# Kernel optimization log

Hardware: AMD Instinct MI355X
Metric: run time of the kernel (lower is better)

## Reference

```python
import jax, jax.numpy as jnp
import numpy as np

B, S, H = 2, 2048, 2304
NH, NKV, HD = 8, 4, 256
SOFTCAP = 50.0
INIT = 0.02


def setup_inputs() -> dict:
    key = jax.random.key(0)
    k1, k2, k3, k4, k5 = jax.random.split(key, 5)
    hidden_states = jax.random.normal(k1, (B, S, H), dtype=jnp.float32)
    attention_mask = jnp.ones((B, S), dtype=jnp.int32)
    position_ids = jnp.broadcast_to(jnp.arange(S, dtype=jnp.int32), (B, S))
    Wq = jax.random.normal(k2, (H, NH * HD), dtype=jnp.float32) * INIT
    Wk = jax.random.normal(k3, (H, NKV * HD), dtype=jnp.float32) * INIT
    Wv = jax.random.normal(k4, (H, NKV * HD), dtype=jnp.float32) * INIT
    Wo = jax.random.normal(k5, (NH * HD, H), dtype=jnp.float32) * INIT
    return {"hidden_states": hidden_states, "attention_mask": attention_mask,
            "position_ids": position_ids, "Wq": Wq, "Wk": Wk, "Wv": Wv, "Wo": Wo}


def _rotate_half(t):
    return jnp.concatenate([-t[..., HD // 2:], t[..., :HD // 2]], axis=-1)


def reference(hidden_states, attention_mask, position_ids, Wq, Wk, Wv, Wo):
    b, s, _ = hidden_states.shape
    # projections + head split
    q = (hidden_states @ Wq).reshape(b, s, NH, HD)
    k = (hidden_states @ Wk).reshape(b, s, NKV, HD)
    v = (hidden_states @ Wv).reshape(b, s, NKV, HD)
    # RoPE (Gemma sinusoidal table, gathered by position_ids)
    inv_freq = 1.0 / (10000.0 ** (jnp.arange(0, HD, 2, dtype=jnp.float32) / HD))
    freqs = position_ids.astype(jnp.float32)[..., None] * inv_freq      # [B,S,HD/2]
    emb = jnp.concatenate([freqs, freqs], axis=-1)                      # [B,S,HD]
    sin = jnp.sin(emb)[:, :, None, :]
    cos = jnp.cos(emb)[:, :, None, :]
    q = q * cos + _rotate_half(q) * sin
    k = k * cos + _rotate_half(k) * sin
    # GQA: repeat KV heads to match query heads
    groups = NH // NKV
    k = jnp.repeat(k, groups, axis=2)
    v = jnp.repeat(v, groups, axis=2)
    # scaled logits, mask, tanh softcap (order matches source: mask -> softcap -> softmax)
    q = q / jnp.sqrt(jnp.float32(HD))
    scores = jnp.einsum('bqhd,bkhd->bhqk', q, k)                        # [B,NH,S,S]
    causal = jnp.tril(jnp.ones((s, s), dtype=bool))
    mask = causal[None, None] & (attention_mask[:, None, None, :] > 0)
    big_neg = jnp.finfo(scores.dtype).min
    scores = jnp.where(mask, scores, big_neg)
    scores = jnp.tanh(scores / SOFTCAP) * SOFTCAP
    w = jax.nn.softmax(scores, axis=-1)
    out = jnp.einsum('bhqk,bkhd->bqhd', w, v).reshape(b, s, NH * HD)
    return out @ Wo
```

## Files before the change

kernel.cpp:

```cpp
#include <hip/hip_runtime.h>
#include <hip/hip_bf16.h>
#include <stdint.h>

typedef unsigned short u16;
typedef __attribute__((ext_vector_type(8))) short s16x8;
typedef __attribute__((ext_vector_type(4))) float f32x4;

#define B_ 2
#define S_ 2048
#define H_ 2304
#define NH_ 8
#define NKV_ 4
#define HD_ 256

__device__ __forceinline__ float bf2f(u16 u) {
  union { uint32_t i; float f; } x; x.i = ((uint32_t)u) << 16; return x.f;
}
__device__ __forceinline__ u16 f2bf(float f) {
  union { float f; uint32_t i; } x; x.f = f;
  uint32_t u = x.i;
  return (u16)((u + 0x7fffu + ((u >> 16) & 1u)) >> 16);
}
__device__ __forceinline__ u16 f2bft(float f) {
  union { float f; uint32_t i; } x; x.f = f;
  return (u16)(x.i >> 16);
}

__device__ __forceinline__ void async16(const void* g, void* l) {
  __builtin_amdgcn_global_load_lds((const __attribute__((address_space(1))) uint32_t*)g,
                                   (__attribute__((address_space(3))) uint32_t*)l, 16, 0, 0);
}

__device__ __forceinline__ f32x4 mfma16(s16x8 a, s16x8 b, f32x4 c) {
  return __builtin_amdgcn_mfma_f32_16x16x32_bf16(a, b, c, 0, 0, 0);
}

__global__ __launch_bounds__(256) void prep_kernel(
    const float* __restrict__ X, u16* __restrict__ Xb,
    const float* __restrict__ Wq, u16* __restrict__ WqT,
    const float* __restrict__ Wk, u16* __restrict__ WkT,
    const float* __restrict__ Wv, u16* __restrict__ WvT,
    const float* __restrict__ Wo, u16* __restrict__ WoT,
    float* __restrict__ ct, float* __restrict__ st) {
  __shared__ u16 tile[32][33];
  int bid = blockIdx.x, tid = threadIdx.x;

  auto tposeT = [&](const float* in, u16* out, int R, int C, int bx, int by) {
    int c0 = bx * 32, r0 = by * 32;
    int x = tid & 31, y = tid >> 5;
#pragma unroll
    for (int j = 0; j < 32; j += 8)
      tile[y + j][x] = f2bf(in[(size_t)(r0 + y + j) * C + c0 + x]);
    __syncthreads();
#pragma unroll
    for (int j = 0; j < 32; j += 8)
      out[(size_t)(c0 + y + j) * R + r0 + x] = tile[x][y + j];
  };

  if (bid < 1024) {
    int t = bid * 256 + tid;
    int d = t & 127;
    int p = t >> 7;
    float invf = exp2f(-(float)d * 0.1038102530f);
    float f = (float)p * invf;
    float s, c;
    sincosf(f, &s, &c);
    ct[t] = c;
    st[t] = s;
  } else if (bid < 10240) {
    size_t i = ((size_t)(bid - 1024) * 256 + tid) * 4;
    float4 v = *(const float4*)(X + i);
    ushort4 o;
    o.x = f2bf(v.x); o.y = f2bf(v.y); o.z = f2bf(v.z); o.w = f2bf(v.w);
    *(ushort4*)(Xb + i) = o;
  } else if (bid < 14848) {
    int b2 = bid - 10240;
    tposeT(Wq, WqT, 2304, 2048, b2 & 63, b2 >> 6);
  } else if (bid < 17152) {
    int b2 = bid - 14848;
    tposeT(Wk, WkT, 2304, 1024, b2 & 31, b2 >> 5);
  } else if (bid < 19456) {
    int b2 = bid - 17152;
    tposeT(Wv, WvT, 2304, 1024, b2 & 31, b2 >> 5);
  } else {
    int b2 = bid - 19456;
    tposeT(Wo, WoT, 2048, 2304, b2 % 72, b2 / 72);
  }
}

__global__ __launch_bounds__(256) void mid_kernel(u16* __restrict__ QKV, u16* __restrict__ VTb,
                                                  const int* __restrict__ pos_ids,
                                                  const float* __restrict__ ct,
                                                  const float* __restrict__ st) {
  __shared__ u16 tile[32][33];
  int bid = blockIdx.x, tid = threadIdx.x;
  if (bid < 1024) {
    int t = bid * 256 + tid;
    int dg = t & 15, h = (t >> 4) & 3, row = t >> 6;
    u16* p1 = QKV + (size_t)row * 4096 + 2048 + h * 256 + dg * 8;
    u16* p2 = p1 + 128;
    int pos = pos_ids[row];
    const float* ctp = ct + pos * 128 + dg * 8;
    const float* stp = st + pos * 128 + dg * 8;
    s16x8 v1 = *(const s16x8*)p1, v2 = *(const s16x8*)p2;
#pragma unroll
    for (int j = 0; j < 8; j++) {
      float c = ctp[j], s = stp[j];
      float a = bf2f((u16)v1[j]);
      float b = bf2f((u16)v2[j]);
      v1[j] = (short)f2bf(a * c - b * s);
      v2[j] = (short)f2bf(b * c + a * s);
    }
    *(s16x8*)p1 = v1;
    *(s16x8*)p2 = v2;
  } else {
    int b2 = bid - 1024;
    int bx = b2 & 31;
    int by = (b2 >> 5) & 63;
    int z = b2 >> 11;
    const u16* in = QKV + 3072 + (size_t)z * 2048 * 4096;
    u16* out = VTb + (size_t)z * 1024 * 2048;
    int c0 = bx * 32, r0 = by * 32;
    int x = tid & 31, y = tid >> 5;
#pragma unroll
    for (int j = 0; j < 32; j += 8)
      tile[y + j][x] = in[(size_t)(r0 + y + j) * 4096 + c0 + x];
    __syncthreads();
#pragma unroll
    for (int j = 0; j < 32; j += 8)
      out[(size_t)(c0 + y + j) * 2048 + r0 + x] = tile[x][y + j];
  }
}

template <bool F32OUT>
__global__ __launch_bounds__(512) void gemm256(const u16* __restrict__ A, const u16* __restrict__ BT,
                                               void* __restrict__ Cout, int M, int N, int Kd) {
  __shared__ u16 As[2][256 * 64];
  __shared__ u16 Bs[2][256 * 64];
  int tid = threadIdx.x, lane = tid & 63, wave = tid >> 6;
  int nT = gridDim.x * gridDim.y;
  int bid = blockIdx.y * gridDim.x + blockIdx.x;
  int tile = (bid & 7) * (nT >> 3) + (bid >> 3);
  int bn = (tile % gridDim.x) * 256;
  int bm = (tile / gridDim.x) * 256;
  int wm = (wave >> 2) * 128, wn = (wave & 3) * 64;
  int fr = lane & 15, fq = lane >> 4;
  f32x4 acc[8][4];
#pragma unroll
  for (int i = 0; i < 8; i++)
#pragma unroll
    for (int j = 0; j < 4; j++) acc[i][j] = (f32x4){0.f, 0.f, 0.f, 0.f};

  int srow = tid >> 3, sslot = tid & 7;
  int scol = (sslot * 8) ^ ((srow & 7) << 3);
  const u16* Ab = A + (size_t)(bm + srow) * Kd + scol;
  const u16* Bb = BT + (size_t)(bn + srow) * Kd + scol;

  auto stage = [&](int buf, int k0) {
#pragma unroll
    for (int i = 0; i < 4; i++) {
      async16(Ab + (size_t)i * 64 * Kd + k0, (char*)&As[buf][0] + wave * 1024 + i * 8192);
      async16(Bb + (size_t)i * 64 * Kd + k0, (char*)&Bs[buf][0] + wave * 1024 + i * 8192);
    }
  };

  int NT = Kd >> 6;
  int rsw = (fr & 7) << 3;
  stage(0, 0);
  for (int t = 0; t < NT; ++t) {
    if (t + 1 < NT) {
      stage((t + 1) & 1, (t + 1) << 6);
      asm volatile("s_waitcnt vmcnt(8)" ::: "memory");
    } else {
      asm volatile("s_waitcnt vmcnt(0)" ::: "memory");
    }
    __builtin_amdgcn_sched_barrier(0);
    __builtin_amdgcn_s_barrier();
    __builtin_amdgcn_sched_barrier(0);
    const u16* Ap = &As[t & 1][0];
    const u16* Bp = &Bs[t & 1][0];
    __builtin_amdgcn_s_setprio(1);
    s16x8 bfr[4][2];
#pragma unroll
    for (int j = 0; j < 4; j++)
#pragma unroll
      for (int s = 0; s < 2; s++)
        bfr[j][s] = *(const s16x8*)&Bp[(wn + j * 16 + fr) * 64 + ((s * 32 + fq * 8) ^ rsw)];
#pragma unroll
    for (int i = 0; i < 8; i++) {
      s16x8 a0 = *(const s16x8*)&Ap[(wm + i * 16 + fr) * 64 + ((fq * 8) ^ rsw)];
      s16x8 a1 = *(const s16x8*)&Ap[(wm + i * 16 + fr) * 64 + ((32 + fq * 8) ^ rsw)];
#pragma unroll
      for (int j = 0; j < 4; j++) {
        acc[i][j] = mfma16(a0, bfr[j][0], acc[i][j]);
        acc[i][j] = mfma16(a1, bfr[j][1], acc[i][j]);
      }
    }
    __builtin_amdgcn_s_setprio(0);
    asm volatile("s_waitcnt lgkmcnt(0)" ::: "memory");
    __builtin_amdgcn_sched_barrier(0);
    __builtin_amdgcn_s_barrier();
  }

#pragma unroll
  for (int i = 0; i < 8; i++)
#pragma unroll
    for (int j = 0; j < 4; j++)
#pragma unroll
      for (int r = 0; r < 4; r++) {
        int row = bm + wm + i * 16 + fq * 4 + r;
        int col = bn + wn + j * 16 + fr;
        if (F32OUT) ((float*)Cout)[(size_t)row * N + col] = acc[i][j][r];
        else        ((u16*)Cout)[(size_t)row * N + col] = f2bf(acc[i][j][r]);
      }
}

template <bool F32OUT>
__global__ __launch_bounds__(256) void gemm128(const u16* __restrict__ A, const u16* __restrict__ BT,
                                               void* __restrict__ Cout, int M, int N, int Kd) {
  __shared__ u16 As[2][128 * 32];
  __shared__ u16 Bs[2][128 * 32];
  int tid = threadIdx.x, lane = tid & 63, wave = tid >> 6;
  int nT = gridDim.x * gridDim.y;
  int bid = blockIdx.y * gridDim.x + blockIdx.x;
  int tile = (bid & 7) * (nT >> 3) + (bid >> 3);
  int bn = (tile % gridDim.x) * 128;
  int bm = (tile / gridDim.x) * 128;
  int wm = (wave >> 1) * 64, wn = (wave & 1) * 64;
  int fr = lane & 15, fq = lane >> 4;
  f32x4 acc[4][4];
#pragma unroll
  for (int i = 0; i < 4; i++)
#pragma unroll
    for (int j = 0; j < 4; j++) acc[i][j] = (f32x4){0.f, 0.f, 0.f, 0.f};

  int srow = tid >> 2, sslot = tid & 3;
  int scol = (sslot * 8) ^ ((srow & 3) << 3);
  const u16* Ab = A + (size_t)(bm + srow) * Kd + scol;
  const u16* Bb = BT + (size_t)(bn + srow) * Kd + scol;

  auto stage = [&](int buf, int k0) {
    async16(Ab + k0, (char*)&As[buf][0] + wave * 1024);
    async16(Ab + (size_t)64 * Kd + k0, (char*)&As[buf][0] + wave * 1024 + 4096);
    async16(Bb + k0, (char*)&Bs[buf][0] + wave * 1024);
    async16(Bb + (size_t)64 * Kd + k0, (char*)&Bs[buf][0] + wave * 1024 + 4096);
  };

  int NT = Kd >> 5;
  int rsw = (fr & 3) << 3;
  stage(0, 0);
  for (int t = 0; t < NT; ++t) {
    if (t + 1 < NT) {
      stage((t + 1) & 1, (t + 1) << 5);
      asm volatile("s_waitcnt vmcnt(4)" ::: "memory");
    } else {
      asm volatile("s_waitcnt vmcnt(0)" ::: "memory");
    }
    __builtin_amdgcn_sched_barrier(0);
    __builtin_amdgcn_s_barrier();
    __builtin_amdgcn_sched_barrier(0);
    const u16* Ap = &As[t & 1][0];
    const u16* Bp = &Bs[t & 1][0];
    __builtin_amdgcn_s_setprio(1);
    s16x8 af[4], bv[4];
#pragma unroll
    for (int i = 0; i < 4; i++) af[i] = *(const s16x8*)&Ap[(wm + i * 16 + fr) * 32 + ((fq * 8) ^ rsw)];
#pragma unroll
    for (int j = 0; j < 4; j++) bv[j] = *(const s16x8*)&Bp[(wn + j * 16 + fr) * 32 + ((fq * 8) ^ rsw)];
#pragma unroll
    for (int i = 0; i < 4; i++)
#pragma unroll
      for (int j = 0; j < 4; j++)
        acc[i][j] = mfma16(af[i], bv[j], acc[i][j]);
    __builtin_amdgcn_s_setprio(0);
    asm volatile("s_waitcnt lgkmcnt(0)" ::: "memory");
    __builtin_amdgcn_sched_barrier(0);
    __builtin_amdgcn_s_barrier();
  }
#pragma unroll
  for (int i = 0; i < 4; i++)
#pragma unroll
    for (int j = 0; j < 4; j++)
#pragma unroll
      for (int r = 0; r < 4; r++) {
        int row = bm + wm + i * 16 + fq * 4 + r;
        int col = bn + wn + j * 16 + fr;
        if (F32OUT) ((float*)Cout)[(size_t)row * N + col] = acc[i][j][r];
        else        ((u16*)Cout)[(size_t)row * N + col] = f2bf(acc[i][j][r]);
      }
}

__global__ __launch_bounds__(256) void attn_kernel(const u16* __restrict__ QKV, const u16* __restrict__ VT,
                                                   const int* __restrict__ amask, const int* __restrict__ pos_ids,
                                                   const float* __restrict__ ct, const float* __restrict__ st,
                                                   u16* __restrict__ O0, u16* __restrict__ O1,
                                                   float* __restrict__ L0, float* __restrict__ L1) {
  __shared__ u16 Kl[2][32 * 256];
  __shared__ u16 Vl[256 * 32];
  __shared__ u16 Pl[4][16 * 32];
  __shared__ unsigned char Mb[256];
  int id = blockIdx.x;
  int bg = id & 7;
  int r_ = id >> 3;
  int qt = 31 - (r_ >> 2);
  int hl = (r_ >> 1) & 1;
  int half = r_ & 1;
  int b = bg >> 2, g = bg & 3;
  int h = g * 2 + hl;
  int tid = threadIdx.x, lane = tid & 63, wave = tid >> 6;
  int fr = lane & 15, fq = lane >> 4;
  int q0 = qt * 64;
  u16* Op = half ? O1 : O0;
  float* Lp = half ? L1 : L0;

  const int* amp = amask + b * S_;
  {
    int4 a = *(const int4*)(amp + tid * 8);
    int4 c = *(const int4*)(amp + tid * 8 + 4);
    unsigned v = (unsigned)(a.x > 0) | ((unsigned)(a.y > 0) << 1) | ((unsigned)(a.z > 0) << 2) |
                 ((unsigned)(a.w > 0) << 3) | ((unsigned)(c.x > 0) << 4) | ((unsigned)(c.y > 0) << 5) |
                 ((unsigned)(c.z > 0) << 6) | ((unsigned)(c.w > 0) << 7);
    Mb[tid] = (unsigned char)v;
  }

  int qrow_g = b * S_ + q0 + wave * 16 + fr;
  s16x8 qr[8];
  const u16* qb = QKV + (size_t)qrow_g * 4096 + h * 256 + fq * 8;
#pragma unroll
  for (int kk = 0; kk < 8; kk++) qr[kk] = *(const s16x8*)(qb + kk * 32);
  int pos = pos_ids[qrow_g];
  const float* ctp = ct + pos * 128 + fq * 8;
  const float* stp = st + pos * 128 + fq * 8;
  s16x8 qf[8];
#pragma unroll
  for (int kk = 0; kk < 4; kk++) {
#pragma unroll
    for (int jj = 0; jj < 8; jj++) {
      float c = ctp[kk * 32 + jj], s = stp[kk * 32 + jj];
      float a = bf2f((u16)qr[kk][jj]);
      float bb = bf2f((u16)qr[kk + 4][jj]);
      qf[kk][jj]     = (short)f2bf((a * c - bb * s) * 0.0625f);
      qf[kk + 4][jj] = (short)f2bf((bb * c + a * s) * 0.0625f);
    }
  }

  f32x4 zero4 = {0.f, 0.f, 0.f, 0.f};
  f32x4 oacc[16];
#pragma unroll
  for (int i = 0; i < 16; i++) oacc[i] = zero4;
  f32x4 lacc = zero4;
  s16x8 onesv;
#pragma unroll
  for (int i = 0; i < 8; i++) onesv[i] = (short)0x3F80;

  const u16* Kbase = QKV + (size_t)b * S_ * 4096 + 2048 + g * 256;
  const u16* Vbase = VT + (size_t)(b * 4 + g) * 256 * S_;

  const u16* KsP[4];
  const u16* VsP[4];
  int dst16[4];
#pragma unroll
  for (int i = 0; i < 4; i++) {
    int c = tid + i * 256;
    int key = c >> 5, slot = c & 31;
    KsP[i] = Kbase + (size_t)key * 4096 + ((slot ^ (key & 7)) * 8);
    int hd = c >> 2, vs = c & 3;
    VsP[i] = Vbase + (size_t)hd * 2048 + ((vs ^ ((hd >> 1) & 3)) * 8);
    dst16[i] = c * 16;
  }

  __syncthreads();

#pragma unroll
  for (int i = 0; i < 4; i++)
    async16(KsP[i] + (size_t)(half * 32) * 4096, (char*)&Kl[0][0] + dst16[i]);

  int nt = 2 * qt + 2;
  int ksw = fr & 7;
  int vswl = (fr >> 1) & 3;
  int psw = (fr & 3) << 3;
  int kb = 0;
  for (int t = half; t < nt; t += 2) {
    int k0 = t * 32;
    bool more = (t + 2 < nt);
    asm volatile("s_waitcnt vmcnt(0)" ::: "memory");
    __builtin_amdgcn_sched_barrier(0);
    __builtin_amdgcn_s_barrier();
    __builtin_amdgcn_sched_barrier(0);

#pragma unroll
    for (int i = 0; i < 4; i++)
      async16(VsP[i] + k0, (char*)&Vl[0] + dst16[i]);
    if (more) {
#pragma unroll
      for (int i = 0; i < 4; i++)
        async16(KsP[i] + (size_t)(k0 + 64) * 4096, (char*)&Kl[kb ^ 1][0] + dst16[i]);
    }

    const u16* Kp = &Kl[kb][0];
    __builtin_amdgcn_s_setprio(1);
    f32x4 s0 = zero4, s1 = zero4;
#pragma unroll
    for (int kk = 0; kk < 8; kk++) {
      s16x8 b0 = *(const s16x8*)&Kp[fr * 256 + (((kk * 4 + fq) ^ ksw) * 8)];
      s16x8 b1 = *(const s16x8*)&Kp[(16 + fr) * 256 + (((kk * 4 + fq) ^ ksw) * 8)];
      s0 = mfma16(qf[kk], b0, s0);
      s1 = mfma16(qf[kk], b1, s1);
    }
    __builtin_amdgcn_s_setprio(0);

    int am0 = (Mb[(k0 + fr) >> 3] >> ((k0 + fr) & 7)) & 1;
    int am1 = (Mb[(k0 + 16 + fr) >> 3] >> ((k0 + 16 + fr) & 7)) & 1;
    bool needmask = (t >= nt - 2);
    float pv0[4], pv1[4];
#pragma unroll
    for (int r = 0; r < 4; r++) {
      float e20 = __expf(s0[r] * 0.04f);
      float e21 = __expf(s1[r] * 0.04f);
      pv0[r] = __expf(__fdividef(-100.f, e20 + 1.f));
      pv1[r] = __expf(__fdividef(-100.f, e21 + 1.f));
    }
    if (needmask) {
#pragma unroll
      for (int r = 0; r < 4; r++) {
        int qg = q0 + wave * 16 + fq * 4 + r;
        if (!((k0 + fr) <= qg)) pv0[r] = 0.f;
        if (!((k0 + 16 + fr) <= qg)) pv1[r] = 0.f;
      }
    }
#pragma unroll
    for (int r = 0; r < 4; r++) {
      int qrow = fq * 4 + r;
      float p0 = am0 ? pv0[r] : 0.f;
      float p1 = am1 ? pv1[r] : 0.f;
      Pl[wave][qrow * 32 + (fr ^ (r << 3))] = f2bft(p0);
      Pl[wave][qrow * 32 + ((16 + fr) ^ (r << 3))] = f2bft(p1);
    }
    asm volatile("s_waitcnt lgkmcnt(0)" ::: "memory");
    __builtin_amdgcn_sched_barrier(0);
    if (more)
      asm volatile("s_waitcnt vmcnt(4)" ::: "memory");
    else
      asm volatile("s_waitcnt vmcnt(0)" ::: "memory");
    __builtin_amdgcn_sched_barrier(0);
    __builtin_amdgcn_s_barrier();
    __builtin_amdgcn_sched_barrier(0);

    s16x8 pf = *(const s16x8*)&Pl[wave][fr * 32 + ((fq * 8) ^ psw)];
    __builtin_amdgcn_s_setprio(1);
    lacc = mfma16(pf, onesv, lacc);
#pragma unroll
    for (int df = 0; df < 16; df++) {
      s16x8 vv = *(const s16x8*)&Vl[(df * 16 + fr) * 32 + ((fq ^ vswl) * 8)];
      oacc[df] = mfma16(pf, vv, oacc[df]);
    }
    __builtin_amdgcn_s_setprio(0);
    asm volatile("s_waitcnt lgkmcnt(0)" ::: "memory");
    __builtin_amdgcn_sched_barrier(0);
    kb ^= 1;
  }

  if (fr == 0) {
#pragma unroll
    for (int r = 0; r < 4; r++)
      Lp[(size_t)(b * S_ + q0 + wave * 16 + fq * 4 + r) * 8 + h] = lacc[r];
  }
#pragma unroll
  for (int df = 0; df < 16; df++) {
#pragma unroll
    for (int r = 0; r < 4; r++) {
      Op[(size_t)(b * S_ + q0 + wave * 16 + fq * 4 + r) * 2048 + h * 256 + df * 16 + fr] =
          f2bf(oacc[df][r]);
    }
  }
}

__global__ void combine_o(const u16* __restrict__ O0, const u16* __restrict__ O1,
                          const float* __restrict__ L0, const float* __restrict__ L1,
                          u16* __restrict__ AO) {
  int idx = blockIdx.x * blockDim.x + threadIdx.x;
  int row = idx >> 8;
  int cg = idx & 255;
  int h = cg >> 5;
  float rinv = 1.0f / (L0[row * 8 + h] + L1[row * 8 + h]);
  size_t base = (size_t)row * 2048 + cg * 8;
  s16x8 a = *(const s16x8*)(O0 + base);
  s16x8 b = *(const s16x8*)(O1 + base);
  s16x8 o;
#pragma unroll
  for (int j = 0; j < 8; j++)
    o[j] = (short)f2bf((bf2f((u16)a[j]) + bf2f((u16)b[j])) * rinv);
  *(s16x8*)(AO + base) = o;
}

extern "C" void kernel_launch(void* const* d_in, const int* in_sizes, int n_in,
                              void* d_out, int out_size, void* d_ws, size_t ws_size,
                              hipStream_t stream) {
  const float* X   = (const float*)d_in[0];
  const int* amask = (const int*)d_in[1];
  const int* pos   = (const int*)d_in[2];
  const float* Wq  = (const float*)d_in[3];
  const float* Wk  = (const float*)d_in[4];
  const float* Wv  = (const float*)d_in[5];
  const float* Wo  = (const float*)d_in[6];
  float* out = (float*)d_out;

  char* ws = (char*)d_ws;
  size_t off = 0;
  auto allocB = [&](size_t bytes) {
    char* p = ws + off;
    off += ((bytes + 255) & ~(size_t)255);
    return p;
  };
  u16* Xb   = (u16*)allocB((size_t)4096 * 2304 * 2);
  u16* WqT  = (u16*)allocB((size_t)2048 * 2304 * 2);
  u16* WkT  = (u16*)allocB((size_t)1024 * 2304 * 2);
  u16* WvT  = (u16*)allocB((size_t)1024 * 2304 * 2);
  u16* WoT  = (u16*)allocB((size_t)2304 * 2048 * 2);
  u16* QKV  = (u16*)allocB((size_t)4096 * 4096 * 2);
  u16* VTb  = (u16*)allocB((size_t)4096 * 1024 * 2);
  u16* AO   = (u16*)allocB((size_t)4096 * 2048 * 2);
  float* CT = (float*)allocB((size_t)2048 * 128 * 4);
  float* ST = (float*)allocB((size_t)2048 * 128 * 4);
  float* Lp0 = (float*)allocB((size_t)4096 * 8 * 4);
  float* Lp1 = (float*)allocB((size_t)4096 * 8 * 4);
  u16* Op0 = (u16*)ws;
  u16* Op1 = Op0 + (size_t)4096 * 2048;
  if (off > ws_size) return;

  prep_kernel<<<24064, 256, 0, stream>>>(X, Xb, Wq, WqT, Wk, WkT, Wv, WvT, Wo, WoT, CT, ST);

  gemm256<false><<<dim3(4096 / 256, 4096 / 256), 512, 0, stream>>>(Xb, WqT, QKV, 4096, 4096, 2304);

  mid_kernel<<<5120, 256, 0, stream>>>(QKV, VTb, pos, CT, ST);

  attn_kernel<<<dim3(1024), 256, 0, stream>>>(QKV, VTb, amask, pos, CT, ST, Op0, Op1, Lp0, Lp1);

  combine_o<<<4096, 256, 0, stream>>>(Op0, Op1, Lp0, Lp1, AO);

  gemm128<true><<<dim3(2304 / 128, 4096 / 128), 256, 0, stream>>>(AO, WoT, out, 4096, 2304, 2048);
}
```

Before: 241.9 us.

## Interleave next-tile global prefetch with MFMA quarters in 256-tile GEMM

Splits the per-K-step MFMA work into four row quarters, each with its own LDS fragment loads and a block barrier. The next tile's async global-to-LDS copies are issued during the first two quarters instead of all at once before compute. The loop now waits for all outstanding loads (vmcnt(0)) at the top of each step. The aim is to spread memory issue across compute and cut scheduling stalls, at the cost of extra barriers per K-step and a shorter prefetch lead time.

New measurement: 240.8 us. About the same (-0.4%).

```diff
diff --git a/kernel.cpp b/kernel.cpp
--- a/kernel.cpp
+++ b/kernel.cpp
@@ -156,50 +156,63 @@
   const u16* Ab = A + (size_t)(bm + srow) * Kd + scol;
   const u16* Bb = BT + (size_t)(bn + srow) * Kd + scol;
 
-  auto stage = [&](int buf, int k0) {
-#pragma unroll
-    for (int i = 0; i < 4; i++) {
+  auto stage1 = [&](int buf, int k0, int i) {
+    if (i < 4)
       async16(Ab + (size_t)i * 64 * Kd + k0, (char*)&As[buf][0] + wave * 1024 + i * 8192);
-      async16(Bb + (size_t)i * 64 * Kd + k0, (char*)&Bs[buf][0] + wave * 1024 + i * 8192);
-    }
+    else
+      async16(Bb + (size_t)(i - 4) * 64 * Kd + k0, (char*)&Bs[buf][0] + wave * 1024 + (i - 4) * 8192);
   };
 
   int NT = Kd >> 6;
   int rsw = (fr & 7) << 3;
-  stage(0, 0);
+#pragma unroll
+  for (int i = 0; i < 8; i++) stage1(0, 0, i);
+
   for (int t = 0; t < NT; ++t) {
-    if (t + 1 < NT) {
-      stage((t + 1) & 1, (t + 1) << 6);
-      asm volatile("s_waitcnt vmcnt(8)" ::: "memory");
-    } else {
-      asm volatile("s_waitcnt vmcnt(0)" ::: "memory");
-    }
+    asm volatile("s_waitcnt vmcnt(0)" ::: "memory");
     __builtin_amdgcn_sched_barrier(0);
     __builtin_amdgcn_s_barrier();
     __builtin_amdgcn_sched_barrier(0);
     const u16* Ap = &As[t & 1][0];
     const u16* Bp = &Bs[t & 1][0];
-    __builtin_amdgcn_s_setprio(1);
+    bool more = (t + 1 < NT);
+    int nb = (t + 1) & 1;
+    int nk = (t + 1) << 6;
     s16x8 bfr[4][2];
 #pragma unroll
-    for (int j = 0; j < 4; j++)
-#pragma unroll
-      for (int s = 0; s < 2; s++)
-        bfr[j][s] = *(const s16x8*)&Bp[(wn + j * 16 + fr) * 64 + ((s * 32 + fq * 8) ^ rsw)];
-#pragma unroll
-    for (int i = 0; i < 8; i++) {
-      s16x8 a0 = *(const s16x8*)&Ap[(wm + i * 16 + fr) * 64 + ((fq * 8) ^ rsw)];
-      s16x8 a1 = *(const s16x8*)&Ap[(wm + i * 16 + fr) * 64 + ((32 + fq * 8) ^ rsw)];
-#pragma unroll
-      for (int j = 0; j < 4; j++) {
-        acc[i][j] = mfma16(a0, bfr[j][0], acc[i][j]);
-        acc[i][j] = mfma16(a1, bfr[j][1], acc[i][j]);
+    for (int q = 0; q < 4; q++) {
+      if (q == 0) {
+#pragma unroll
+        for (int j = 0; j < 4; j++)
+#pragma unroll
+          for (int s = 0; s < 2; s++)
+            bfr[j][s] = *(const s16x8*)&Bp[(wn + j * 16 + fr) * 64 + ((s * 32 + fq * 8) ^ rsw)];
       }
-    }
-    __builtin_amdgcn_s_setprio(0);
-    asm volatile("s_waitcnt lgkmcnt(0)" ::: "memory");
-    __builtin_amdgcn_sched_barrier(0);
-    __builtin_amdgcn_s_barrier();
+      s16x8 aq[2][2];
+#pragma unroll
+      for (int rf = 0; rf < 2; rf++)
+#pragma unroll
+        for (int s = 0; s < 2; s++)
+          aq[rf][s] = *(const s16x8*)&Ap[(wm + q * 32 + rf * 16 + fr) * 64 + ((s * 32 + fq * 8) ^ rsw)];
+      if (more && q < 2) {
+#pragma unroll
+        for (int i = 0; i < 4; i++) stage1(nb, nk, q * 4 + i);
+      }
+      asm volatile("s_waitcnt lgkmcnt(0)" ::: "memory");
+      __builtin_amdgcn_sched_barrier(0);
+      __builtin_amdgcn_s_setprio(1);
+#pragma unroll
+      for (int rf = 0; rf < 2; rf++)
+#pragma unroll
+        for (int j = 0; j < 4; j++) {
+          acc[q * 2 + rf][j] = mfma16(aq[rf][0], bfr[j][0], acc[q * 2 + rf][j]);
+          acc[q * 2 + rf][j] = mfma16(aq[rf][1], bfr[j][1], acc[q * 2 + rf][j]);
+        }
+      __builtin_amdgcn_s_setprio(0);
+      __builtin_amdgcn_sched_barrier(0);
+      __builtin_amdgcn_s_barrier();
+      __builtin_amdgcn_sched_barrier(0);
+    }
   }
 
 #pragma unroll
```
